# Performance work log

Measured on AMD Instinct MI355X. Metric: run time of the kernel, lower is better.

Reference implementation:

```python
import jax, jax.numpy as jnp
import numpy as np

N_NODES = 50000
N_EDGES = 800000
FEAT_DIM = 1024
EMBED_DIM = 128


def setup_inputs() -> dict:
    key = jax.random.key(0)
    k_x, k_w, k_r, k_c, k_v = jax.random.split(key, 5)
    x = jax.random.normal(k_x, (N_NODES, FEAT_DIM), dtype=jnp.float32)
    # xavier-uniform equivalent for weight [embed_dim, feat_dim]
    limit = float(np.sqrt(6.0 / (EMBED_DIM + FEAT_DIM)))
    weight = jax.random.uniform(k_w, (EMBED_DIM, FEAT_DIM), dtype=jnp.float32,
                                minval=-limit, maxval=limit)
    # sparse adjacency in COO form (row = destination, col = source)
    adj_row = jax.random.randint(k_r, (N_EDGES,), 0, N_NODES, dtype=jnp.int32)
    adj_col = jax.random.randint(k_c, (N_EDGES,), 0, N_NODES, dtype=jnp.int32)
    adj_vals = jax.random.uniform(k_v, (N_EDGES,), dtype=jnp.float32)
    return {"x": x, "weight": weight, "adj_row": adj_row,
            "adj_col": adj_col, "adj_vals": adj_vals}


def reference(x, weight, adj_row, adj_col, adj_vals):
    # Fused GeMM-SpMM: out = A @ (x @ W^T)
    h = jnp.einsum('nf,ef->ne', x, weight)          # [N, embed_dim] dense GEMM
    msgs = adj_vals[:, None] * h[adj_col]           # gather source rows, scale by edge weight
    out = jax.ops.segment_sum(msgs, adj_row, num_segments=N_NODES)  # scatter-add to dest rows
    return out
```

## Files before the change

### kernel.cpp

```cpp
#include <hip/hip_runtime.h>
#include <hip/hip_bf16.h>

#define FEAT 1024
#define EMBED 128
#define CAP 64
#define OVF_CAP 4096

typedef __attribute__((ext_vector_type(8))) short short8;
typedef __attribute__((ext_vector_type(4))) float floatx4;

__device__ inline ushort f2bf(float f) {
    __hip_bfloat16 h = __float2bfloat16(f);
    return *reinterpret_cast<ushort*>(&h);
}
__device__ inline float bfbits_lo(uint u) {
    uint v = u << 16; return *reinterpret_cast<float*>(&v);
}
__device__ inline float bfbits_hi(uint u) {
    uint v = u & 0xffff0000u; return *reinterpret_cast<float*>(&v);
}

__global__ void swizzle_weight_kernel(const float* __restrict__ w,
                                      ushort* __restrict__ wbs) {
    int gid = blockIdx.x * blockDim.x + threadIdx.x;
    int l = gid & 63;
    int t = (gid >> 6) & 7;
    int s = gid >> 9;
    int row = t * 16 + (l & 15);
    int col = s * 32 + (l >> 4) * 8;
    const float* src = w + (size_t)row * FEAT + col;
    float4 v0 = *(const float4*)(src);
    float4 v1 = *(const float4*)(src + 4);
    short8 o;
    o[0] = f2bf(v0.x); o[1] = f2bf(v0.y); o[2] = f2bf(v0.z); o[3] = f2bf(v0.w);
    o[4] = f2bf(v1.x); o[5] = f2bf(v1.y); o[6] = f2bf(v1.z); o[7] = f2bf(v1.w);
    *(short8*)(wbs + (size_t)gid * 8) = o;
}

__launch_bounds__(128, 3)
__global__ void gemm_xwT_kernel(const float* __restrict__ x,
                                const ushort* __restrict__ wbs,
                                ushort* __restrict__ hb, int n_nodes) {
    const int lane = threadIdx.x & 63;
    const int wave = threadIdx.x >> 6;
    const int q    = lane >> 4;
    const int m    = lane & 15;
    const int base = blockIdx.x * 64 + wave * 32;

    int row0 = base + m;
    int row1 = base + 16 + m;
    int r0l = row0 < n_nodes ? row0 : (n_nodes - 1);
    int r1l = row1 < n_nodes ? row1 : (n_nodes - 1);
    const float*  xp0 = x + (size_t)r0l * FEAT + q * 8;
    const float*  xp1 = x + (size_t)r1l * FEAT + q * 8;
    const ushort* bp  = wbs + lane * 8;

    floatx4 acc[2][8];
#pragma unroll
    for (int rf = 0; rf < 2; ++rf)
#pragma unroll
        for (int t = 0; t < 8; ++t) acc[rf][t] = (floatx4)(0.0f);

    float4 a00 = *(const float4*)(xp0);
    float4 a01 = *(const float4*)(xp0 + 4);
    float4 a10 = *(const float4*)(xp1);
    float4 a11 = *(const float4*)(xp1 + 4);

    for (int s = 0; s < 32; ++s) {
        float4 n00, n01, n10, n11;
        if (s < 31) {
            n00 = *(const float4*)(xp0 + (s + 1) * 32);
            n01 = *(const float4*)(xp0 + (s + 1) * 32 + 4);
            n10 = *(const float4*)(xp1 + (s + 1) * 32);
            n11 = *(const float4*)(xp1 + (s + 1) * 32 + 4);
        }
        const ushort* bs = bp + s * 4096;
        short8 bf[8];
#pragma unroll
        for (int t = 0; t < 8; ++t) bf[t] = *(const short8*)(bs + t * 512);

        short8 af0, af1;
        af0[0] = f2bf(a00.x); af0[1] = f2bf(a00.y);
        af0[2] = f2bf(a00.z); af0[3] = f2bf(a00.w);
        af0[4] = f2bf(a01.x); af0[5] = f2bf(a01.y);
        af0[6] = f2bf(a01.z); af0[7] = f2bf(a01.w);
        af1[0] = f2bf(a10.x); af1[1] = f2bf(a10.y);
        af1[2] = f2bf(a10.z); af1[3] = f2bf(a10.w);
        af1[4] = f2bf(a11.x); af1[5] = f2bf(a11.y);
        af1[6] = f2bf(a11.z); af1[7] = f2bf(a11.w);

#pragma unroll
        for (int t = 0; t < 8; ++t) {
            acc[0][t] = __builtin_amdgcn_mfma_f32_16x16x32_bf16(af0, bf[t], acc[0][t], 0, 0, 0);
            acc[1][t] = __builtin_amdgcn_mfma_f32_16x16x32_bf16(af1, bf[t], acc[1][t], 0, 0, 0);
        }
        a00 = n00; a01 = n01; a10 = n10; a11 = n11;
    }

#pragma unroll
    for (int rf = 0; rf < 2; ++rf) {
#pragma unroll
        for (int t = 0; t < 8; ++t) {
#pragma unroll
            for (int r = 0; r < 4; ++r) {
                int rr = base + rf * 16 + q * 4 + r;
                if (rr < n_nodes)
                    hb[(size_t)rr * EMBED + t * 16 + m] = f2bf(acc[rf][t][r]);
            }
        }
    }
}

__global__ void bucket_fill_kernel(const int* __restrict__ adj_row,
                                   const int* __restrict__ adj_col,
                                   const float* __restrict__ adj_vals,
                                   int* __restrict__ cnt,
                                   int2* __restrict__ bucket,
                                   int* __restrict__ ovf_cnt,
                                   int* __restrict__ ovf_list,
                                   int n_edges) {
    int e = blockIdx.x * blockDim.x + threadIdx.x;
    if (e >= n_edges) return;
    int r = adj_row[e];
    int slot = atomicAdd(&cnt[r], 1);
    if (slot < CAP) {
        bucket[(size_t)r * CAP + slot] = make_int2(adj_col[e], __float_as_int(adj_vals[e]));
    } else {
        int oi = atomicAdd(ovf_cnt, 1);
        if (oi < OVF_CAP) ovf_list[oi] = e;
    }
}

__launch_bounds__(256)
__global__ void gather_kernel(const int* __restrict__ cnt,
                              const int2* __restrict__ bucket,
                              const ushort* __restrict__ hb,
                              float* __restrict__ out, int n_nodes) {
    int node = __builtin_amdgcn_readfirstlane(blockIdx.x * 4 + (threadIdx.x >> 6));
    if (node >= n_nodes) return;
    int lane = threadIdx.x & 63;
    int c = cnt[node];
    if (c > CAP) c = CAP;
    const int2* bp = bucket + (size_t)node * CAP;
    const ushort* hl = hb + lane * 2;

    float accx = 0.0f, accy = 0.0f;
    int j = 0;
    for (; j + 8 <= c; j += 8) {
        int4 e01 = *(const int4*)(bp + j);
        int4 e23 = *(const int4*)(bp + j + 2);
        int4 e45 = *(const int4*)(bp + j + 4);
        int4 e67 = *(const int4*)(bp + j + 6);
        uint u0 = *(const uint*)(hl + (size_t)e01.x * EMBED);
        uint u1 = *(const uint*)(hl + (size_t)e01.z * EMBED);
        uint u2 = *(const uint*)(hl + (size_t)e23.x * EMBED);
        uint u3 = *(const uint*)(hl + (size_t)e23.z * EMBED);
        uint u4 = *(const uint*)(hl + (size_t)e45.x * EMBED);
        uint u5 = *(const uint*)(hl + (size_t)e45.z * EMBED);
        uint u6 = *(const uint*)(hl + (size_t)e67.x * EMBED);
        uint u7 = *(const uint*)(hl + (size_t)e67.z * EMBED);
        float w0 = __int_as_float(e01.y), w1 = __int_as_float(e01.w);
        float w2 = __int_as_float(e23.y), w3 = __int_as_float(e23.w);
        float w4 = __int_as_float(e45.y), w5 = __int_as_float(e45.w);
        float w6 = __int_as_float(e67.y), w7 = __int_as_float(e67.w);
        accx = fmaf(w0, bfbits_lo(u0), accx);  accy = fmaf(w0, bfbits_hi(u0), accy);
        accx = fmaf(w1, bfbits_lo(u1), accx);  accy = fmaf(w1, bfbits_hi(u1), accy);
        accx = fmaf(w2, bfbits_lo(u2), accx);  accy = fmaf(w2, bfbits_hi(u2), accy);
        accx = fmaf(w3, bfbits_lo(u3), accx);  accy = fmaf(w3, bfbits_hi(u3), accy);
        accx = fmaf(w4, bfbits_lo(u4), accx);  accy = fmaf(w4, bfbits_hi(u4), accy);
        accx = fmaf(w5, bfbits_lo(u5), accx);  accy = fmaf(w5, bfbits_hi(u5), accy);
        accx = fmaf(w6, bfbits_lo(u6), accx);  accy = fmaf(w6, bfbits_hi(u6), accy);
        accx = fmaf(w7, bfbits_lo(u7), accx);  accy = fmaf(w7, bfbits_hi(u7), accy);
    }
    for (; j + 2 <= c; j += 2) {
        int4 e01 = *(const int4*)(bp + j);
        uint u0 = *(const uint*)(hl + (size_t)e01.x * EMBED);
        uint u1 = *(const uint*)(hl + (size_t)e01.z * EMBED);
        float w0 = __int_as_float(e01.y), w1 = __int_as_float(e01.w);
        accx = fmaf(w0, bfbits_lo(u0), accx);  accy = fmaf(w0, bfbits_hi(u0), accy);
        accx = fmaf(w1, bfbits_lo(u1), accx);  accy = fmaf(w1, bfbits_hi(u1), accy);
    }
    if (j < c) {
        int2 ev = bp[j];
        uint u = *(const uint*)(hl + (size_t)ev.x * EMBED);
        float w = __int_as_float(ev.y);
        accx = fmaf(w, bfbits_lo(u), accx);
        accy = fmaf(w, bfbits_hi(u), accy);
    }
    *(float2*)(out + (size_t)node * EMBED + lane * 2) = make_float2(accx, accy);
}

__global__ void overflow_fixup_kernel(const int* __restrict__ ovf_cnt,
                                      const int* __restrict__ ovf_list,
                                      const int* __restrict__ adj_row,
                                      const int* __restrict__ adj_col,
                                      const float* __restrict__ adj_vals,
                                      const ushort* __restrict__ hb,
                                      float* __restrict__ out) {
    int n = *ovf_cnt;
    if (n > OVF_CAP) n = OVF_CAP;
    int f = threadIdx.x;
    for (int i = blockIdx.x; i < n; i += gridDim.x) {
        int e = ovf_list[i];
        uint us = hb[(size_t)adj_col[e] * EMBED + f];
        uint v = us << 16;
        atomicAdd(&out[(size_t)adj_row[e] * EMBED + f],
                  adj_vals[e] * *reinterpret_cast<float*>(&v));
    }
}

extern "C" void kernel_launch(void* const* d_in, const int* in_sizes, int n_in,
                              void* d_out, int out_size, void* d_ws, size_t ws_size,
                              hipStream_t stream) {
    const float* x        = (const float*)d_in[0];
    const float* w        = (const float*)d_in[1];
    const int*   adj_row  = (const int*)d_in[2];
    const int*   adj_col  = (const int*)d_in[3];
    const float* adj_vals = (const float*)d_in[4];

    const int n_nodes = in_sizes[0] / FEAT;
    const int n_edges = in_sizes[2];
    float* out = (float*)d_out;

    char* ws = (char*)d_ws;
    ushort* wbs = (ushort*)ws;
    size_t off = 262144;
    ushort* hb = (ushort*)(ws + off);
    off += (size_t)n_nodes * EMBED * sizeof(ushort);
    char* meta = ws + off;
    int* cnt      = (int*)meta;
    int* ovf_cnt  = (int*)(meta + (size_t)n_nodes * 4);
    int* ovf_list = ovf_cnt + 1;
    size_t meta_bytes = ((size_t)n_nodes * 4 + 4 + OVF_CAP * 4 + 15) & ~(size_t)15;
    int2* bucket = (int2*)(meta + meta_bytes);

    hipMemsetAsync(meta, 0, meta_bytes, stream);

    swizzle_weight_kernel<<<64, 256, 0, stream>>>(w, wbs);

    gemm_xwT_kernel<<<(n_nodes + 63) / 64, 128, 0, stream>>>(x, wbs, hb, n_nodes);

    bucket_fill_kernel<<<(n_edges + 255) / 256, 256, 0, stream>>>(
        adj_row, adj_col, adj_vals, cnt, bucket, ovf_cnt, ovf_list, n_edges);

    gather_kernel<<<(n_nodes + 3) / 4, 256, 0, stream>>>(cnt, bucket, hb, out, n_nodes);

    overflow_fixup_kernel<<<64, 128, 0, stream>>>(
        ovf_cnt, ovf_list, adj_row, adj_col, adj_vals, hb, out);
}
```

Measured before the change: 408.5 us.

## Stage swizzled weight tiles in LDS with async double-buffered copies

The GEMM kernel now copies each chunk of the pre-swizzled bf16 weight into double-buffered LDS using global_load_lds async copies, and reads the B fragments from LDS. Before, every wave reloaded them from global memory or cache. Blocks grow to 4 waves and 128 rows so four waves share each staged chunk. The x rows are prefetched four k-steps at a time in registers. This cuts redundant global weight traffic but adds a barrier per chunk, uses 64KB of LDS per block, and raises register pressure, which may limit occupancy.

```diff
diff --git a/kernel.cpp b/kernel.cpp
--- a/kernel.cpp
+++ b/kernel.cpp
@@ -18,6 +18,12 @@
 }
 __device__ inline float bfbits_hi(uint u) {
     uint v = u & 0xffff0000u; return *reinterpret_cast<float*>(&v);
+}
+
+__device__ inline void async_copy16(const void* g, void* l) {
+    __builtin_amdgcn_global_load_lds(
+        (const __attribute__((address_space(1))) void*)g,
+        (__attribute__((address_space(3))) void*)l, 16, 0, 0);
 }
 
 __global__ void swizzle_weight_kernel(const float* __restrict__ w,
@@ -37,23 +43,45 @@
     *(short8*)(wbs + (size_t)gid * 8) = o;
 }
 
-__launch_bounds__(128, 3)
+__launch_bounds__(256, 2)
 __global__ void gemm_xwT_kernel(const float* __restrict__ x,
                                 const ushort* __restrict__ wbs,
                                 ushort* __restrict__ hb, int n_nodes) {
+    __shared__ ushort lds[2][16384];
+
     const int lane = threadIdx.x & 63;
     const int wave = threadIdx.x >> 6;
     const int q    = lane >> 4;
     const int m    = lane & 15;
-    const int base = blockIdx.x * 64 + wave * 32;
+    const int base = blockIdx.x * 128 + wave * 32;
 
     int row0 = base + m;
     int row1 = base + 16 + m;
     int r0l = row0 < n_nodes ? row0 : (n_nodes - 1);
     int r1l = row1 < n_nodes ? row1 : (n_nodes - 1);
-    const float*  xp0 = x + (size_t)r0l * FEAT + q * 8;
-    const float*  xp1 = x + (size_t)r1l * FEAT + q * 8;
-    const ushort* bp  = wbs + lane * 8;
+    const float* xp0 = x + (size_t)r0l * FEAT + q * 8;
+    const float* xp1 = x + (size_t)r1l * FEAT + q * 8;
+
+    const char* wb = (const char*)wbs;
+    const size_t stage_src_off = (size_t)(wave * 8 * 64 + lane) * 16;
+    const int    stage_dst_off = wave * 8192;
+
+    {
+        const char* src = wb + stage_src_off;
+        char* dst = (char*)lds[0] + stage_dst_off;
+#pragma unroll
+        for (int k = 0; k < 8; ++k)
+            async_copy16(src + k * 1024, dst + k * 1024);
+    }
+
+    float4 A[4][4];
+#pragma unroll
+    for (int u = 0; u < 4; ++u) {
+        A[u][0] = *(const float4*)(xp0 + u * 32);
+        A[u][1] = *(const float4*)(xp0 + u * 32 + 4);
+        A[u][2] = *(const float4*)(xp1 + u * 32);
+        A[u][3] = *(const float4*)(xp1 + u * 32 + 4);
+    }
 
     floatx4 acc[2][8];
 #pragma unroll
@@ -61,40 +89,52 @@
 #pragma unroll
         for (int t = 0; t < 8; ++t) acc[rf][t] = (floatx4)(0.0f);
 
-    float4 a00 = *(const float4*)(xp0);
-    float4 a01 = *(const float4*)(xp0 + 4);
-    float4 a10 = *(const float4*)(xp1);
-    float4 a11 = *(const float4*)(xp1 + 4);
-
-    for (int s = 0; s < 32; ++s) {
-        float4 n00, n01, n10, n11;
-        if (s < 31) {
-            n00 = *(const float4*)(xp0 + (s + 1) * 32);
-            n01 = *(const float4*)(xp0 + (s + 1) * 32 + 4);
-            n10 = *(const float4*)(xp1 + (s + 1) * 32);
-            n11 = *(const float4*)(xp1 + (s + 1) * 32 + 4);
+    __syncthreads();
+
+    for (int c = 0; c < 8; ++c) {
+        const ushort* buf = lds[c & 1];
+        if (c < 7) {
+            const char* src = wb + (size_t)(c + 1) * 32768 + stage_src_off;
+            char* dst = (char*)lds[(c + 1) & 1] + stage_dst_off;
+#pragma unroll
+            for (int k = 0; k < 8; ++k)
+                async_copy16(src + k * 1024, dst + k * 1024);
         }
-        const ushort* bs = bp + s * 4096;
-        short8 bf[8];
-#pragma unroll
-        for (int t = 0; t < 8; ++t) bf[t] = *(const short8*)(bs + t * 512);
-
-        short8 af0, af1;
-        af0[0] = f2bf(a00.x); af0[1] = f2bf(a00.y);
-        af0[2] = f2bf(a00.z); af0[3] = f2bf(a00.w);
-        af0[4] = f2bf(a01.x); af0[5] = f2bf(a01.y);
-        af0[6] = f2bf(a01.z); af0[7] = f2bf(a01.w);
-        af1[0] = f2bf(a10.x); af1[1] = f2bf(a10.y);
-        af1[2] = f2bf(a10.z); af1[3] = f2bf(a10.w);
-        af1[4] = f2bf(a11.x); af1[5] = f2bf(a11.y);
-        af1[6] = f2bf(a11.z); af1[7] = f2bf(a11.w);
-
-#pragma unroll
-        for (int t = 0; t < 8; ++t) {
-            acc[0][t] = __builtin_amdgcn_mfma_f32_16x16x32_bf16(af0, bf[t], acc[0][t], 0, 0, 0);
-            acc[1][t] = __builtin_amdgcn_mfma_f32_16x16x32_bf16(af1, bf[t], acc[1][t], 0, 0, 0);
+#pragma unroll
+        for (int u = 0; u < 4; ++u) {
+            const ushort* bs = buf + u * 4096 + lane * 8;
+            short8 bf[8];
+#pragma unroll
+            for (int t = 0; t < 8; ++t) bf[t] = *(const short8*)(bs + t * 512);
+
+            short8 af0, af1;
+            af0[0] = f2bf(A[u][0].x); af0[1] = f2bf(A[u][0].y);
+            af0[2] = f2bf(A[u][0].z); af0[3] = f2bf(A[u][0].w);
+            af0[4] = f2bf(A[u][1].x); af0[5] = f2bf(A[u][1].y);
+            af0[6] = f2bf(A[u][1].z); af0[7] = f2bf(A[u][1].w);
+            af1[0] = f2bf(A[u][2].x); af1[1] = f2bf(A[u][2].y);
+            af1[2] = f2bf(A[u][2].z); af1[3] = f2bf(A[u][2].w);
+            af1[4] = f2bf(A[u][3].x); af1[5] = f2bf(A[u][3].y);
+            af1[6] = f2bf(A[u][3].z); af1[7] = f2bf(A[u][3].w);
+
+            if (u == 3 && c < 7) {
+                const float* p0 = xp0 + (c + 1) * 128;
+                const float* p1 = xp1 + (c + 1) * 128;
+#pragma unroll
+                for (int uu = 0; uu < 4; ++uu) {
+                    A[uu][0] = *(const float4*)(p0 + uu * 32);
+                    A[uu][1] = *(const float4*)(p0 + uu * 32 + 4);
+                    A[uu][2] = *(const float4*)(p1 + uu * 32);
+                    A[uu][3] = *(const float4*)(p1 + uu * 32 + 4);
+                }
+            }
+#pragma unroll
+            for (int t = 0; t < 8; ++t) {
+                acc[0][t] = __builtin_amdgcn_mfma_f32_16x16x32_bf16(af0, bf[t], acc[0][t], 0, 0, 0);
+                acc[1][t] = __builtin_amdgcn_mfma_f32_16x16x32_bf16(af1, bf[t], acc[1][t], 0, 0, 0);
+            }
         }
-        a00 = n00; a01 = n01; a10 = n10; a11 = n11;
+        __syncthreads();
     }
 
 #pragma unroll
@@ -238,7 +278,7 @@
 
     swizzle_weight_kernel<<<64, 256, 0, stream>>>(w, wbs);
 
-    gemm_xwT_kernel<<<(n_nodes + 63) / 64, 128, 0, stream>>>(x, wbs, hb, n_nodes);
+    gemm_xwT_kernel<<<(n_nodes + 127) / 128, 256, 0, stream>>>(x, wbs, hb, n_nodes);
 
     bucket_fill_kernel<<<(n_edges + 255) / 256, 256, 0, stream>>>(
         adj_row, adj_col, adj_vals, cnt, bucket, ovf_cnt, ovf_list, n_edges);
```

Result: faster. 390.8 us (-4.3%).
